# Kernel tuning notes

Hardware: AMD Instinct MI355X
Metric: run time of the kernel (lower is better)

## Reference

```python
import jax, jax.numpy as jnp
import numpy as np

DIM = 1024
NUM_HEADS = 16
HEAD_DIM = DIM // NUM_HEADS


def setup_inputs() -> dict:
    key = jax.random.key(0)
    ks = jax.random.split(key, 5)
    x = jax.random.normal(ks[0], (2, 4096, DIM), dtype=jnp.float32)
    # nn.Linear(dim, 3*dim): weight [3D, D], bias [3D]; we store transposed [D, 3D]
    scale = 1.0 / np.sqrt(DIM)
    w_qkv = jax.random.normal(ks[1], (DIM, 3 * DIM), dtype=jnp.float32) * scale
    b_qkv = jax.random.normal(ks[2], (3 * DIM,), dtype=jnp.float32) * scale
    w_o = jax.random.normal(ks[3], (DIM, DIM), dtype=jnp.float32) * scale
    b_o = jax.random.normal(ks[4], (DIM,), dtype=jnp.float32) * scale
    return {"x": x, "w_qkv": w_qkv, "b_qkv": b_qkv, "w_o": w_o, "b_o": b_o}


def reference(x, w_qkv, b_qkv, w_o, b_o):
    b, n, _ = x.shape
    h, d = NUM_HEADS, HEAD_DIM
    qkv = x @ w_qkv + b_qkv                      # [B, N, 3D]
    q, k, v = jnp.split(qkv, 3, axis=-1)
    # [B, N, H, d] -> [B, H, N, d]
    q = q.reshape(b, n, h, d).transpose(0, 2, 1, 3)
    k = k.reshape(b, n, h, d).transpose(0, 2, 1, 3)
    v = v.reshape(b, n, h, d).transpose(0, 2, 1, 3)
    scale = 1.0 / np.sqrt(d).astype(np.float32)
    score = jnp.einsum("bhqd,bhkd->bhqk", q, k) * scale   # [B, H, N, N]
    attn = jax.nn.softmax(score, axis=-1)
    out = jnp.einsum("bhqk,bhkd->bhqd", attn, v)          # [B, H, N, d]
    out = out.transpose(0, 2, 1, 3).reshape(b, n, h * d)  # [B, N, D]
    return out @ w_o + b_o
```

## Files before the change

kernel.cpp:

```cpp
#include <hip/hip_runtime.h>

typedef __attribute__((ext_vector_type(8))) __bf16 bf16x8;
typedef __attribute__((ext_vector_type(8))) short short8;
typedef __attribute__((ext_vector_type(4))) float f32x4;
typedef __attribute__((ext_vector_type(2))) unsigned int uint32x2;

#define C_LOG2E 0.1803368801111183f
#define M_LOG2  11.541560327111707f

__device__ __forceinline__ unsigned short f2bf(float f) {
    union { float f; unsigned int i; } c; c.f = f;
    unsigned int r = c.i + 0x7fffu + ((c.i >> 16) & 1u);
    return (unsigned short)(r >> 16);
}

__device__ __forceinline__ unsigned int cvt_pk_bf16(float lo, float hi) {
    unsigned int r;
    asm("v_cvt_pk_bf16_f32 %0, %1, %2" : "=v"(r) : "v"(lo), "v"(hi));
    return r;
}

__device__ __forceinline__ bf16x8 pack_bf16x8(unsigned int a, unsigned int b,
                                              unsigned int c, unsigned int d) {
    union { unsigned int u[4]; bf16x8 v; } x;
    x.u[0] = a; x.u[1] = b; x.u[2] = c; x.u[3] = d;
    return x.v;
}

#if __has_builtin(__builtin_amdgcn_exp2f)
#define FAST_EXP2(x) __builtin_amdgcn_exp2f(x)
#else
#define FAST_EXP2(x) __expf((x) * 0.6931471805599453f)
#endif

__device__ __forceinline__ void async_cp16(const unsigned short* g, unsigned short* l) {
    __builtin_amdgcn_global_load_lds(
        (const __attribute__((address_space(1))) unsigned int*)g,
        (__attribute__((address_space(3))) unsigned int*)l, 16, 0, 0);
}

#define DIM 1024
#define NSEQ 4096
#define NH 16
#define HD 64

#define SWZ(row, col) (((row) << 6) + ((col) ^ (((row) & 7) << 3)))

__global__ __launch_bounds__(256)
void conv_kernel(const float* __restrict__ in, unsigned short* __restrict__ out)
{
    const int i = blockIdx.x * 256 + threadIdx.x;
    const float4 a0 = ((const float4*)in)[i * 2];
    const float4 a1 = ((const float4*)in)[i * 2 + 1];
    short8 v;
    v[0] = (short)f2bf(a0.x); v[1] = (short)f2bf(a0.y);
    v[2] = (short)f2bf(a0.z); v[3] = (short)f2bf(a0.w);
    v[4] = (short)f2bf(a1.x); v[5] = (short)f2bf(a1.y);
    v[6] = (short)f2bf(a1.z); v[7] = (short)f2bf(a1.w);
    ((short8*)out)[i] = v;
}

template<int N, int K>
__global__ __launch_bounds__(256)
void transpose_conv_kernel(const float* __restrict__ in, unsigned short* __restrict__ out)
{
    __shared__ unsigned short Ls[64][65];
    const int t  = threadIdx.x;
    const int k0 = blockIdx.x * 64, n0 = blockIdx.y * 64;
    const int kl = t >> 2, nl = (t & 3) * 16;
    const float* src = in + (size_t)(k0 + kl) * N + n0 + nl;
    #pragma unroll
    for (int i = 0; i < 4; i++) {
        float4 a = *(const float4*)(src + i * 4);
        Ls[kl][nl + i*4 + 0] = f2bf(a.x); Ls[kl][nl + i*4 + 1] = f2bf(a.y);
        Ls[kl][nl + i*4 + 2] = f2bf(a.z); Ls[kl][nl + i*4 + 3] = f2bf(a.w);
    }
    __syncthreads();
    const int kl2 = (t & 7) * 8;
    #pragma unroll
    for (int i = 0; i < 2; i++) {
        const int nl2 = (t >> 3) + i * 32;
        short8 v;
        #pragma unroll
        for (int j = 0; j < 8; j++) v[j] = (short)Ls[kl2 + j][nl2];
        *(short8*)(out + (size_t)(n0 + nl2) * K + k0 + kl2) = v;
    }
}

template<int MODE>
__global__ __launch_bounds__(256)
void gemm_kernel(const unsigned short* __restrict__ A,
                 const unsigned short* __restrict__ Bt,
                 const float* __restrict__ bias,
                 unsigned short* __restrict__ out0,
                 unsigned short* __restrict__ out1,
                 unsigned short* __restrict__ out2,
                 float* __restrict__ outf)
{
    __shared__ __align__(16) unsigned short AsBs[2][128][32];
    unsigned short (&As)[128][32] = AsBs[0];
    unsigned short (&Bs)[128][32] = AsBs[1];
    const int t    = threadIdx.x;
    const int m0   = blockIdx.x * 128, n0 = blockIdx.y * 128;
    const int lane = t & 63, wv = t >> 6;
    const int l15  = lane & 15, quad = lane >> 4;
    const int wm   = (wv >> 1) * 64, wn = (wv & 1) * 64;
    const int sr   = wv * 16 + (lane >> 2);
    const int sc   = (lane & 3) * 8;
    const unsigned short* Ag = A  + (size_t)m0 * 1024;
    const unsigned short* Bg = Bt + (size_t)n0 * 1024;

    f32x4 acc[4][4] = {};

    for (int kt = 0; kt < 1024; kt += 32) {
        __syncthreads();
        async_cp16(Ag + (size_t)(sr)      * 1024 + kt + sc, &As[sr][sc]);
        async_cp16(Ag + (size_t)(sr + 64) * 1024 + kt + sc, &As[sr + 64][sc]);
        async_cp16(Bg + (size_t)(sr)      * 1024 + kt + sc, &Bs[sr][sc]);
        async_cp16(Bg + (size_t)(sr + 64) * 1024 + kt + sc, &Bs[sr + 64][sc]);
        __syncthreads();

        bf16x8 af[4], bfr[4];
        #pragma unroll
        for (int mi = 0; mi < 4; mi++) af[mi]  = *(const bf16x8*)&As[wm + mi*16 + l15][quad*8];
        #pragma unroll
        for (int ni = 0; ni < 4; ni++) bfr[ni] = *(const bf16x8*)&Bs[wn + ni*16 + l15][quad*8];
        #pragma unroll
        for (int mi = 0; mi < 4; mi++)
            #pragma unroll
            for (int ni = 0; ni < 4; ni++)
                acc[mi][ni] = __builtin_amdgcn_mfma_f32_16x16x32_bf16(af[mi], bfr[ni], acc[mi][ni], 0, 0, 0);
    }

    if (MODE == 0 && n0 >= 2048) {
        unsigned short (*Tb)[130] = (unsigned short (*)[130])&AsBs[0][0][0];
        const int hbase = (n0 - 2048) >> 6;
        const int bb = m0 >> 12, ns0 = m0 & 4095;
        const int dd = t >> 2, seg = (t & 3) * 32;
        #pragma unroll
        for (int p = 0; p < 2; p++) {
            __syncthreads();
            if ((wv & 1) == p) {
                #pragma unroll
                for (int mi = 0; mi < 4; mi++) {
                    #pragma unroll
                    for (int ni = 0; ni < 4; ni++) {
                        const int colL = ni*16 + l15;
                        const float bval = bias[n0 + p*64 + colL];
                        #pragma unroll
                        for (int r = 0; r < 4; r++) {
                            const int row = wm + mi*16 + quad*4 + r;
                            Tb[colL][row] = f2bf(acc[mi][ni][r] + bval);
                        }
                    }
                }
            }
            __syncthreads();
            const size_t obase =
                ((size_t)((bb * NH + hbase + p) * HD + dd)) * NSEQ + ns0 + seg;
            #pragma unroll
            for (int j = 0; j < 4; j++)
                *(short8*)(out2 + obase + j*8) = *(const short8*)&Tb[dd][seg + j*8];
        }
        return;
    }

    #pragma unroll
    for (int mi = 0; mi < 4; mi++) {
        #pragma unroll
        for (int ni = 0; ni < 4; ni++) {
            const int col  = n0 + wn + ni*16 + l15;
            const float bval = bias[col];
            #pragma unroll
            for (int r = 0; r < 4; r++) {
                const int row = m0 + wm + mi*16 + quad*4 + r;
                const float val = acc[mi][ni][r] + bval;
                if (MODE == 0) {
                    const int which = col >> 10;
                    const int rem   = col & 1023;
                    const int h = rem >> 6, dd = rem & 63;
                    const int bb = row >> 12, ns = row & 4095;
                    const size_t off = ((size_t)((bb * NH + h) * NSEQ + ns)) * HD + dd;
                    if (which == 0) out0[off] = f2bf(val * C_LOG2E);
                    else            out1[off] = f2bf(val);
                } else {
                    outf[(size_t)row * 1024 + col] = val;
                }
            }
        }
    }
}

__global__ __launch_bounds__(256, 4)
void attn_kernel(const unsigned short* __restrict__ qb,
                 const unsigned short* __restrict__ kb,
                 const unsigned short* __restrict__ vb,
                 unsigned short* __restrict__ ob)
{
    __shared__ __align__(16) unsigned short Ks[2][64 * 64];
    __shared__ __align__(16) unsigned short Vt[2][64 * 64];

    const int t    = threadIdx.x;
    const int wv   = t >> 6, lane = t & 63, l15 = lane & 15, quad = lane >> 4;
    const int q0   = blockIdx.x * 128;
    const int h    = blockIdx.y, b = blockIdx.z;
    const size_t bh = (size_t)(b * NH + h) * NSEQ * HD;
    const unsigned short* Qp  = qb + bh;
    const unsigned short* Kp  = kb + bh;
    const unsigned short* Vtp = vb + bh;

    bf16x8 aq[2][2];
    #pragma unroll
    for (int mi = 0; mi < 2; mi++) {
        const unsigned short* qrow =
            Qp + (size_t)(q0 + wv*32 + mi*16 + l15) * HD + quad*8;
        aq[mi][0] = *(const bf16x8*)(qrow);
        aq[mi][1] = *(const bf16x8*)(qrow + 32);
    }

    const bf16x8 ones8 = pack_bf16x8(0x3F803F80u, 0x3F803F80u,
                                     0x3F803F80u, 0x3F803F80u);
    const f32x4 minit = {-M_LOG2, -M_LOG2, -M_LOG2, -M_LOG2};

    f32x4 acc_l[2] = {};
    f32x4 acc_o[2][4] = {};

    const int srow = lane >> 3;
    const int sg8  = ((lane & 7) ^ srow) * 8;
    const int rA   = wv * 16 + srow;
    const int rB   = rA + 8;
    unsigned short* ldsKA0 = &Ks[0][(wv*16 + 0) * 64];
    unsigned short* ldsKB0 = &Ks[0][(wv*16 + 8) * 64];
    unsigned short* ldsVA0 = &Vt[0][(wv*16 + 0) * 64];
    unsigned short* ldsVB0 = &Vt[0][(wv*16 + 8) * 64];
    unsigned short* ldsKA1 = &Ks[1][(wv*16 + 0) * 64];
    unsigned short* ldsKB1 = &Ks[1][(wv*16 + 8) * 64];
    unsigned short* ldsVA1 = &Vt[1][(wv*16 + 0) * 64];
    unsigned short* ldsVB1 = &Vt[1][(wv*16 + 8) * 64];

    async_cp16(Kp  + (size_t)rA * HD + sg8,   ldsKA0);
    async_cp16(Kp  + (size_t)rB * HD + sg8,   ldsKB0);
    async_cp16(Vtp + (size_t)rA * NSEQ + sg8, ldsVA0);
    async_cp16(Vtp + (size_t)rB * NSEQ + sg8, ldsVB0);

    int cur = 0;
    for (int kt = 0; kt < NSEQ; kt += 64) {
        __syncthreads();

        if (kt + 64 < NSEQ) {
            const int ktn = kt + 64;
            async_cp16(Kp  + (size_t)(ktn + rA) * HD + sg8, cur ? ldsKA0 : ldsKA1);
            async_cp16(Kp  + (size_t)(ktn + rB) * HD + sg8, cur ? ldsKB0 : ldsKB1);
            async_cp16(Vtp + (size_t)rA * NSEQ + ktn + sg8, cur ? ldsVA0 : ldsVA1);
            async_cp16(Vtp + (size_t)rB * NSEQ + ktn + sg8, cur ? ldsVB0 : ldsVB1);
        }

        const unsigned short* Kc = Ks[cur];
        const unsigned short* Vc = Vt[cur];

        f32x4 accs[2][4];
        #pragma unroll
        for (int mi = 0; mi < 2; mi++)
            #pragma unroll
            for (int nj = 0; nj < 4; nj++)
                accs[mi][nj] = minit;
        __builtin_amdgcn_s_setprio(1);
        #pragma unroll
        for (int nj = 0; nj < 4; nj++) {
            bf16x8 bk0 = *(const bf16x8*)&Kc[SWZ(nj*16 + l15, quad*8)];
            bf16x8 bk1 = *(const bf16x8*)&Kc[SWZ(nj*16 + l15, 32 + quad*8)];
            #pragma unroll
            for (int mi = 0; mi < 2; mi++) {
                accs[mi][nj] = __builtin_amdgcn_mfma_f32_16x16x32_bf16(bk0, aq[mi][0], accs[mi][nj], 0, 0, 0);
                accs[mi][nj] = __builtin_amdgcn_mfma_f32_16x16x32_bf16(bk1, aq[mi][1], accs[mi][nj], 0, 0, 0);
            }
        }
        __builtin_amdgcn_s_setprio(0);

        uint2 pw[2][4];
        #pragma unroll
        for (int mi = 0; mi < 2; mi++) {
            #pragma unroll
            for (int nj = 0; nj < 4; nj++) {
                const float p0 = FAST_EXP2(accs[mi][nj][0]);
                const float p1 = FAST_EXP2(accs[mi][nj][1]);
                const float p2 = FAST_EXP2(accs[mi][nj][2]);
                const float p3 = FAST_EXP2(accs[mi][nj][3]);
                pw[mi][nj].x = cvt_pk_bf16(p0, p1);
                pw[mi][nj].y = cvt_pk_bf16(p2, p3);
            }
        }

        bf16x8 apf[2][2];
        #pragma unroll
        for (int mi = 0; mi < 2; mi++)
            #pragma unroll
            for (int W = 0; W < 2; W++)
                apf[mi][W] = pack_bf16x8(pw[mi][2*W].x,   pw[mi][2*W].y,
                                         pw[mi][2*W+1].x, pw[mi][2*W+1].y);

        __builtin_amdgcn_s_setprio(1);
        #pragma unroll
        for (int mi = 0; mi < 2; mi++) {
            acc_l[mi] = __builtin_amdgcn_mfma_f32_16x16x32_bf16(apf[mi][0], ones8, acc_l[mi], 0, 0, 0);
            acc_l[mi] = __builtin_amdgcn_mfma_f32_16x16x32_bf16(apf[mi][1], ones8, acc_l[mi], 0, 0, 0);
        }

        #pragma unroll
        for (int njd = 0; njd < 4; njd++) {
            const int drow = njd * 16 + l15;
            #pragma unroll
            for (int W = 0; W < 2; W++) {
                const uint32x2 lo = *(const uint32x2*)&Vc[SWZ(drow, W*32 + quad*4)];
                const uint32x2 hi = *(const uint32x2*)&Vc[SWZ(drow, W*32 + 16 + quad*4)];
                const bf16x8 bv = pack_bf16x8(lo[0], lo[1], hi[0], hi[1]);
                #pragma unroll
                for (int mi = 0; mi < 2; mi++) {
                    acc_o[mi][njd] = __builtin_amdgcn_mfma_f32_16x16x32_bf16(apf[mi][W], bv, acc_o[mi][njd], 0, 0, 0);
                }
            }
        }
        __builtin_amdgcn_s_setprio(0);

        cur ^= 1;
    }

    #pragma unroll
    for (int mi = 0; mi < 2; mi++) {
        #pragma unroll
        for (int r = 0; r < 4; r++) {
            const float inv = 1.0f / acc_l[mi][r];
            const int row = q0 + wv*32 + mi*16 + quad*4 + r;
            const size_t base = ((size_t)(b * NSEQ + row)) * DIM + h * HD;
            #pragma unroll
            for (int nj = 0; nj < 4; nj++)
                ob[base + nj*16 + l15] = f2bf(acc_o[mi][nj][r] * inv);
        }
    }
}

extern "C" void kernel_launch(void* const* d_in, const int* in_sizes, int n_in,
                              void* d_out, int out_size, void* d_ws, size_t ws_size,
                              hipStream_t stream)
{
    const float *x = nullptr, *w_qkv = nullptr, *b_qkv = nullptr,
                *w_o = nullptr, *b_o = nullptr;
    for (int i = 0; i < n_in; i++) {
        switch (in_sizes[i]) {
            case 8388608: x     = (const float*)d_in[i]; break;
            case 3145728: w_qkv = (const float*)d_in[i]; break;
            case 3072:    b_qkv = (const float*)d_in[i]; break;
            case 1048576: w_o   = (const float*)d_in[i]; break;
            case 1024:    b_o   = (const float*)d_in[i]; break;
        }
    }
    float* out = (float*)d_out;

    const size_t WQB  = (size_t)3072 * 1024;
    const size_t WOB  = (size_t)1024 * 1024;
    const size_t SEGB = (size_t)NSEQ * DIM;

    char* p = (char*)d_ws;
    unsigned short* wqb = (unsigned short*)p;  p += WQB * 2;
    unsigned short* wob = (unsigned short*)p;  p += WOB * 2;

    transpose_conv_kernel<3072, 1024><<<dim3(16, 48), 256, 0, stream>>>(w_qkv, wqb);
    transpose_conv_kernel<1024, 1024><<<dim3(16, 16), 256, 0, stream>>>(w_o, wob);

    const size_t tier1_bytes = (WQB + WOB + 2*SEGB + 3*2*SEGB) * 2;
    if (ws_size >= tier1_bytes) {
        unsigned short* xb = (unsigned short*)p;  p += 2 * SEGB * 2;
        unsigned short* qb = (unsigned short*)p;  p += 2 * SEGB * 2;
        unsigned short* kb = (unsigned short*)p;  p += 2 * SEGB * 2;
        unsigned short* vb = (unsigned short*)p;
        unsigned short* ao = xb;
        conv_kernel<<<4096, 256, 0, stream>>>(x, xb);
        gemm_kernel<0><<<dim3(64, 24), 256, 0, stream>>>(xb, wqb, b_qkv, qb, kb, vb, nullptr);
        attn_kernel<<<dim3(32, NH, 2), 256, 0, stream>>>(qb, kb, vb, ao);
        gemm_kernel<1><<<dim3(64, 8), 256, 0, stream>>>(ao, wob, b_o, nullptr, nullptr, nullptr, out);
    } else {
        unsigned short* xb = (unsigned short*)p;  p += SEGB * 2;
        unsigned short* qb = (unsigned short*)p;  p += SEGB * 2;
        unsigned short* kb = (unsigned short*)p;  p += SEGB * 2;
        unsigned short* vb = (unsigned short*)p;
        unsigned short* ao = xb;
        for (int b = 0; b < 2; b++) {
            conv_kernel<<<2048, 256, 0, stream>>>(x + b * SEGB, xb);
            gemm_kernel<0><<<dim3(32, 24), 256, 0, stream>>>(xb, wqb, b_qkv, qb, kb, vb, nullptr);
            attn_kernel<<<dim3(32, NH, 1), 256, 0, stream>>>(qb, kb, vb, ao);
            gemm_kernel<1><<<dim3(32, 8), 256, 0, stream>>>(ao, wob, b_o, nullptr, nullptr, nullptr, out + b * SEGB);
        }
    }
}
```

Before: 341.7 us.

## Double GEMM K-tile to 64 with XOR-swizzled LDS layout

Raises the GEMM k-step from 32 to 64 elements per LDS stage, which halves the number of barrier pairs across the K loop. The shared-memory tile is stored with an XOR column swizzle, and the fragment loads read through SWZ, to cut LDS bank conflicts on the wider rows. Each stage now issues four 16-byte async copies per operand per thread and runs two MFMA sub-steps. The cost is doubled LDS use per block, which could lower occupancy, and the change depends on a SWZ helper being defined elsewhere in the file.

```diff
diff --git a/kernel.cpp b/kernel.cpp
--- a/kernel.cpp
+++ b/kernel.cpp
@@ -97,43 +97,51 @@
                  unsigned short* __restrict__ out2,
                  float* __restrict__ outf)
 {
-    __shared__ __align__(16) unsigned short AsBs[2][128][32];
-    unsigned short (&As)[128][32] = AsBs[0];
-    unsigned short (&Bs)[128][32] = AsBs[1];
+    __shared__ __align__(16) unsigned short AsBs[2][128 * 64];
+    unsigned short* As = AsBs[0];
+    unsigned short* Bs = AsBs[1];
     const int t    = threadIdx.x;
     const int m0   = blockIdx.x * 128, n0 = blockIdx.y * 128;
     const int lane = t & 63, wv = t >> 6;
     const int l15  = lane & 15, quad = lane >> 4;
     const int wm   = (wv >> 1) * 64, wn = (wv & 1) * 64;
-    const int sr   = wv * 16 + (lane >> 2);
-    const int sc   = (lane & 3) * 8;
+
+    const int srow8 = t >> 3;
+    const int scol  = (((t & 7) ^ (srow8 & 7)) * 8);
+    const int sdst  = t * 8;
     const unsigned short* Ag = A  + (size_t)m0 * 1024;
     const unsigned short* Bg = Bt + (size_t)n0 * 1024;
 
     f32x4 acc[4][4] = {};
 
-    for (int kt = 0; kt < 1024; kt += 32) {
+    for (int kt = 0; kt < 1024; kt += 64) {
         __syncthreads();
-        async_cp16(Ag + (size_t)(sr)      * 1024 + kt + sc, &As[sr][sc]);
-        async_cp16(Ag + (size_t)(sr + 64) * 1024 + kt + sc, &As[sr + 64][sc]);
-        async_cp16(Bg + (size_t)(sr)      * 1024 + kt + sc, &Bs[sr][sc]);
-        async_cp16(Bg + (size_t)(sr + 64) * 1024 + kt + sc, &Bs[sr + 64][sc]);
+        #pragma unroll
+        for (int j = 0; j < 4; j++) {
+            async_cp16(Ag + (size_t)(j*32 + srow8) * 1024 + kt + scol, &As[j*2048 + sdst]);
+            async_cp16(Bg + (size_t)(j*32 + srow8) * 1024 + kt + scol, &Bs[j*2048 + sdst]);
+        }
         __syncthreads();
 
-        bf16x8 af[4], bfr[4];
-        #pragma unroll
-        for (int mi = 0; mi < 4; mi++) af[mi]  = *(const bf16x8*)&As[wm + mi*16 + l15][quad*8];
-        #pragma unroll
-        for (int ni = 0; ni < 4; ni++) bfr[ni] = *(const bf16x8*)&Bs[wn + ni*16 + l15][quad*8];
-        #pragma unroll
-        for (int mi = 0; mi < 4; mi++)
+        #pragma unroll
+        for (int h = 0; h < 2; h++) {
+            bf16x8 af[4], bfr[4];
+            #pragma unroll
+            for (int mi = 0; mi < 4; mi++)
+                af[mi]  = *(const bf16x8*)&As[SWZ(wm + mi*16 + l15, h*32 + quad*8)];
             #pragma unroll
             for (int ni = 0; ni < 4; ni++)
-                acc[mi][ni] = __builtin_amdgcn_mfma_f32_16x16x32_bf16(af[mi], bfr[ni], acc[mi][ni], 0, 0, 0);
+                bfr[ni] = *(const bf16x8*)&Bs[SWZ(wn + ni*16 + l15, h*32 + quad*8)];
+            #pragma unroll
+            for (int mi = 0; mi < 4; mi++)
+                #pragma unroll
+                for (int ni = 0; ni < 4; ni++)
+                    acc[mi][ni] = __builtin_amdgcn_mfma_f32_16x16x32_bf16(af[mi], bfr[ni], acc[mi][ni], 0, 0, 0);
+        }
     }
 
     if (MODE == 0 && n0 >= 2048) {
-        unsigned short (*Tb)[130] = (unsigned short (*)[130])&AsBs[0][0][0];
+        unsigned short (*Tb)[130] = (unsigned short (*)[130])&AsBs[0][0];
         const int hbase = (n0 - 2048) >> 6;
         const int bb = m0 >> 12, ns0 = m0 & 4095;
         const int dd = t >> 2, seg = (t & 3) * 32;
```

After: 335.9 us. No clear change (-1.7%).
